# Kernel optimization log

Measured on AMD Instinct MI355X. Metric: run time of the kernel, lower is better.

Reference implementation:

```python
import jax, jax.numpy as jnp
import numpy as np

KH = KW = 3
K = KH * KW
MAX_S, MIN_S = 3.0, 0.5
A_S = (MAX_S - MIN_S) / 2.0   # 1.25
B_S = (MAX_S + MIN_S) / 2.0   # 1.75


def _conv3x3(x, w, b):
    # x: [B,C,H,W], w: [O,C,3,3], b: [O]
    y = jax.lax.conv_general_dilated(
        x, w, window_strides=(1, 1), padding='SAME',
        dimension_numbers=('NCHW', 'OIHW', 'NCHW'))
    return y + b[None, :, None, None]


def setup_inputs() -> dict:
    key = jax.random.key(0)
    ks = jax.random.split(key, 6)
    b, c_in, c_out, h, w = 2, 64, 64, 192, 192
    x = jax.random.normal(ks[0], (b, c_in, h, w), jnp.float32)
    w_main = jax.random.normal(ks[1], (c_out, c_in, KH, KW), jnp.float32) * 0.05
    # offset-branch params (randomized, small, so offsets are non-trivial)
    w_rot = jax.random.normal(ks[2], (2, c_in, 3, 3), jnp.float32) * 0.05
    b_rot = jnp.array([0.0, 1.0], jnp.float32)  # init_angle=0 -> (sin,cos)=(0,1)
    w_str = jax.random.normal(ks[3], (1, c_in, 3, 3), jnp.float32) * 0.05
    b_str = jnp.zeros((1,), jnp.float32)
    w_whole = jax.random.normal(ks[4], (1, c_in, 3, 3), jnp.float32) * 0.05
    b_whole = jnp.zeros((1,), jnp.float32)
    return dict(x=x, w_main=w_main, w_rot=w_rot, b_rot=b_rot,
                w_str=w_str, b_str=b_str, w_whole=w_whole, b_whole=b_whole)


def reference(x, w_main, w_rot, b_rot, w_str, b_str, w_whole, b_whole):
    bsz, cin, H, W = x.shape
    # base kernel offsets (row-major over 3x3, centered): di rows, dj cols
    di = jnp.array([-1, -1, -1, 0, 0, 0, 1, 1, 1], jnp.float32)  # [K]
    dj = jnp.array([-1, 0, 1, -1, 0, 1, -1, 0, 1], jnp.float32)  # [K]

    # per-pixel rotation (normalized sin/cos)
    rot = _conv3x3(x, w_rot, b_rot)          # [B,2,H,W]
    sin, cos = rot[:, 0], rot[:, 1]          # [B,H,W]
    norm = jnp.sqrt(sin * sin + cos * cos + 1e-6)
    sin, cos = sin / norm, cos / norm

    # stretch on the row coordinate, bounded by tanh into [MIN_S, MAX_S]
    r = jnp.tanh(_conv3x3(x, w_str, b_str))[:, 0] * A_S + B_S   # [B,H,W]
    # whole-grid rescale >= 1
    wr = 1.0 + jax.nn.relu(_conv3x3(x, w_whole, b_whole))[:, 0]  # [B,H,W]

    # banded offsets before rotation: row comp scaled by r*wr, col by wr
    bd0 = di * (r * wr)[..., None]           # [B,H,W,K]
    bd1 = dj * wr[..., None]                 # [B,H,W,K]
    # rotation matrix [[cos, sin], [-sin, cos]] @ [bd0; bd1], minus base
    off_y = cos[..., None] * bd0 + sin[..., None] * bd1 - di     # [B,H,W,K]
    off_x = -sin[..., None] * bd0 + cos[..., None] * bd1 - dj    # [B,H,W,K]

    # sampling positions: p = out_pos - pad + tap + offset; (tap - pad) == di/dj
    py = jnp.arange(H, dtype=jnp.float32)[None, :, None, None] + di + off_y
    px = jnp.arange(W, dtype=jnp.float32)[None, None, :, None] + dj + off_x

    # bilinear gather with zero padding outside the image
    x_bhwc = x.transpose(0, 2, 3, 1)         # [B,H,W,C]
    y0 = jnp.floor(py)
    x0 = jnp.floor(px)
    ty = py - y0
    tx = px - x0
    y0i = y0.astype(jnp.int32)
    x0i = x0.astype(jnp.int32)
    bidx = jnp.arange(bsz)[:, None, None, None]

    def gather(yi, xi):
        valid = ((yi >= 0) & (yi < H) & (xi >= 0) & (xi < W)).astype(x.dtype)
        v = x_bhwc[bidx, jnp.clip(yi, 0, H - 1), jnp.clip(xi, 0, W - 1)]  # [B,H,W,K,C]
        return v * valid[..., None]

    sampled = (gather(y0i, x0i) * ((1 - ty) * (1 - tx))[..., None]
               + gather(y0i, x0i + 1) * ((1 - ty) * tx)[..., None]
               + gather(y0i + 1, x0i) * (ty * (1 - tx))[..., None]
               + gather(y0i + 1, x0i + 1) * (ty * tx)[..., None])  # [B,H,W,K,C]

    w_flat = w_main.reshape(w_main.shape[0], w_main.shape[1], K)   # [O,C,K]
    out = jnp.einsum('bhwkc,ock->bohw', sampled, w_flat)
    return out
```

## Files before the change

kernel.cpp:

```cpp
#include <hip/hip_runtime.h>
#include <hip/hip_bf16.h>
#include <stdint.h>

typedef unsigned short u16;
typedef unsigned int   u32;

#define HH 192
#define WW 192
#define HWSZ (192*192)
#define NPIX (2*HWSZ)
#define NTILE 1152
#define TPB   144

typedef __attribute__((ext_vector_type(8))) short short8;
typedef __attribute__((ext_vector_type(4))) float floatx4;

__device__ __forceinline__ float bflo(u32 u){ union{u32 i; float f;} v; v.i = u<<16; return v.f; }
__device__ __forceinline__ float bfhi(u32 u){ union{u32 i; float f;} v; v.i = u & 0xffff0000u; return v.f; }
__device__ __forceinline__ float bf2f(u16 u){ union{u32 i; float f;} v; v.i = ((u32)u)<<16; return v.f; }
__device__ __forceinline__ u16 f2bf(float f){
    union{float f; u32 i;} v; v.f = f;
    u32 b = v.i;
    u32 r = b + 0x7fffu + ((b>>16)&1u);
    return (u16)(r>>16);
}
__device__ __forceinline__ u32 pkbf(float a, float b){
    __hip_bfloat162 h = __float22bfloat162_rn(make_float2(a, b));
    union { __hip_bfloat162 h; u32 u; } cv; cv.h = h; return cv.u;
}

__device__ __forceinline__ int band_tile(int blk){ return (blk & 7)*TPB + (blk >> 3); }

__device__ __forceinline__ int sniff_fp32(const void* x) {
    const u32* x32 = (const u32*)x;
    int l = threadIdx.x & 63;
    u32 v = x32[l*2];
    u32 e = (v >> 7) & 0xFFu;
    int vote = (e >= 0x60u && e <= 0x8Fu) ? 1 : 0;
    unsigned long long m = __ballot(vote);
    return (__popcll(m) < 40) ? 1 : 0;
}

__device__ __forceinline__ u16 pick16(const void* p, int i, int fp32) {
    return fp32 ? f2bf(((const float*)p)[i]) : ((const u16*)p)[i];
}
__device__ __forceinline__ float pickf(const void* p, int i, int fp32) {
    return fp32 ? ((const float*)p)[i] : bf2f(((const u16*)p)[i]);
}

__global__ __launch_bounds__(256) void k0_prep(const void* __restrict__ x,
                        const void* __restrict__ wm,
                        const void* __restrict__ wrot,
                        const void* __restrict__ brot,
                        const void* __restrict__ wstr,
                        const void* __restrict__ bstr,
                        const void* __restrict__ wwh,
                        const void* __restrict__ bwh,
                        u16* __restrict__ bfrag, float* __restrict__ wf) {
    int fp32 = sniff_fp32(x);
    int e = blockIdx.x*256 + threadIdx.x;
    if (e < 9*2*4*64*8) {
        int j    = e & 7;
        int lane = (e>>3) & 63;
        int wd   = (e>>9) & 3;
        int kk   = (e>>11) & 1;
        int k    = e>>12;
        int o = wd*16 + (lane & 15);
        int c = kk*32 + ((lane>>4)&3)*8 + j;
        bfrag[e] = pick16(wm, (o*64 + c)*9 + k, fp32);
    }
    if (e < 9216) {
        int j   = e & 3;
        int rem = e >> 2;
        int tap = rem % 9;
        int c   = rem / 9;
        float s;
        if (j==0)      s = pickf(wrot, c*9 + tap, fp32);
        else if (j==1) s = pickf(wrot, (64+c)*9 + tap, fp32);
        else if (j==2) s = pickf(wstr, c*9 + tap, fp32);
        else           s = pickf(wwh,  c*9 + tap, fp32);
        wf[e] = s;
    }
    if (e < 4) {
        float bv;
        if (e==0)      bv = pickf(brot, 0, fp32);
        else if (e==1) bv = pickf(brot, 1, fp32);
        else if (e==2) bv = pickf(bstr, 0, fp32);
        else           bv = pickf(bwh,  0, fp32);
        wf[9216 + e] = bv;
    }
}

__global__ __launch_bounds__(256) void k1_transpose(const void* __restrict__ x, u16* __restrict__ xt) {
    int fp32 = sniff_fp32(x);
    int t = threadIdx.x;
    int g = t >> 6, p = t & 63;
    int tile = band_tile(blockIdx.x);
    int gp = tile*64 + p;
    int b = gp / HWSZ, hw = gp % HWSZ;
    u32 v[8];
    if (fp32) {
        const float* src = (const float*)x + (size_t)(b*64 + g*16)*HWSZ + hw;
#pragma unroll
        for (int i = 0; i < 8; i++) {
            float a = src[(size_t)(2*i)*HWSZ];
            float c = src[(size_t)(2*i+1)*HWSZ];
            v[i] = pkbf(a, c);
        }
    } else {
        const u16* src = (const u16*)x + (size_t)(b*64 + g*16)*HWSZ + hw;
#pragma unroll
        for (int i = 0; i < 8; i++) {
            u32 a = src[(size_t)(2*i)*HWSZ];
            u32 c = src[(size_t)(2*i+1)*HWSZ];
            v[i] = a | (c<<16);
        }
    }
    uint4* dst = (uint4*)(xt + (size_t)gp*64 + g*16);
    dst[0] = make_uint4(v[0], v[1], v[2], v[3]);
    dst[1] = make_uint4(v[4], v[5], v[6], v[7]);
}

__global__ __launch_bounds__(256) void k2_fields(const void* __restrict__ x, const float* __restrict__ wf,
                          float4* __restrict__ fields) {
    __shared__ float4 red[256];
    int fp32 = sniff_fp32(x);
    int t = threadIdx.x;
    int q = t >> 6, p = t & 63;
    int gp0 = band_tile(blockIdx.x) * 64;
    int gp = gp0 + p;
    int b = gp / HWSZ, hw = gp % HWSZ;
    int h = hw / WW, w = hw % WW;
    float a0=0.f, a1=0.f, a2=0.f, a3=0.f;
    const float4* wf4 = (const float4*)wf;
    if (fp32) {
        const float* xf = (const float*)x;
#pragma unroll 2
        for (int c16 = 0; c16 < 16; c16++) {
            int c = q*16 + c16;
            size_t plane = (size_t)(b*64 + c)*HWSZ;
#pragma unroll
            for (int kh = 0; kh < 3; kh++) {
                int y = h + kh - 1;
                if ((unsigned)y >= (unsigned)HH) continue;
#pragma unroll
                for (int kw = 0; kw < 3; kw++) {
                    int xx = w + kw - 1;
                    if ((unsigned)xx >= (unsigned)WW) continue;
                    float v = xf[plane + (size_t)y*WW + xx];
                    float4 wv = wf4[c*9 + kh*3 + kw];
                    a0 = fmaf(v, wv.x, a0);
                    a1 = fmaf(v, wv.y, a1);
                    a2 = fmaf(v, wv.z, a2);
                    a3 = fmaf(v, wv.w, a3);
                }
            }
        }
    } else {
        const u16* xu = (const u16*)x;
#pragma unroll 2
        for (int c16 = 0; c16 < 16; c16++) {
            int c = q*16 + c16;
            size_t plane = (size_t)(b*64 + c)*HWSZ;
#pragma unroll
            for (int kh = 0; kh < 3; kh++) {
                int y = h + kh - 1;
                if ((unsigned)y >= (unsigned)HH) continue;
#pragma unroll
                for (int kw = 0; kw < 3; kw++) {
                    int xx = w + kw - 1;
                    if ((unsigned)xx >= (unsigned)WW) continue;
                    float v = bf2f(xu[plane + (size_t)y*WW + xx]);
                    float4 wv = wf4[c*9 + kh*3 + kw];
                    a0 = fmaf(v, wv.x, a0);
                    a1 = fmaf(v, wv.y, a1);
                    a2 = fmaf(v, wv.z, a2);
                    a3 = fmaf(v, wv.w, a3);
                }
            }
        }
    }
    red[t] = make_float4(a0, a1, a2, a3);
    __syncthreads();
    if (t < 64) {
        float4 r0 = red[t], r1 = red[t+64], r2 = red[t+128], r3 = red[t+192];
        float s0 = r0.x + r1.x + r2.x + r3.x;
        float s1 = r0.y + r1.y + r2.y + r3.y;
        float s2 = r0.z + r1.z + r2.z + r3.z;
        float s3 = r0.w + r1.w + r2.w + r3.w;
        float sr = s0 + wf[9216];
        float cr = s1 + wf[9217];
        float inv = 1.0f / sqrtf(sr*sr + cr*cr + 1e-6f);
        float r  = tanhf(s2 + wf[9218])*1.25f + 1.75f;
        float wrv = 1.0f + fmaxf(s3 + wf[9219], 0.0f);
        fields[gp0 + t] = make_float4(sr*inv, cr*inv, r*wrv, wrv);
    }
}

__device__ __forceinline__ void load16(const u16* base, u32 r[8]) {
    const uint4* p = (const uint4*)base;
    uint4 a = p[0], b = p[1];
    r[0]=a.x; r[1]=a.y; r[2]=a.z; r[3]=a.w;
    r[4]=b.x; r[5]=b.y; r[6]=b.z; r[7]=b.w;
}

__global__ __launch_bounds__(256) void k3_main(const void* __restrict__ xorig,
                                               const u16* __restrict__ xt,
                                               const float4* __restrict__ fields,
                                               const u16* __restrict__ bfrag,
                                               void* __restrict__ out) {
    __shared__ u16 samp[2][64*72];

    int fp32 = sniff_fp32(xorig);
    int t = threadIdx.x;
    int pix0 = band_tile(blockIdx.x) * 64;
    int b   = pix0 / HWSZ;
    int hw0 = pix0 % HWSZ;

    int p = t >> 2, q = t & 3;
    int hw = hw0 + p;
    int h = hw / WW, w = hw % WW;
    float4 f = fields[pix0 + p];
    float sn = f.x, cs = f.y, rwr = f.z, wr = f.w;
    const u16* xbase = xt + (size_t)b*HWSZ*64;

    int wd = t >> 6, lane = t & 63;
    int quad = lane >> 4, l15 = lane & 15;
    floatx4 acc[4];
#pragma unroll
    for (int i=0;i<4;i++) acc[i] = (floatx4){0.f,0.f,0.f,0.f};
    const short8* bfr = (const short8*)bfrag;

    u32 r00[8], r01[8], r10[8], r11[8];
    float w00, w01, w10, w11;

    auto coords_load = [&](int k) {
        int di = k/3 - 1;
        int dj = k%3 - 1;
        float bd0 = (float)di * rwr;
        float bd1 = (float)dj * wr;
        float py = (float)h + cs*bd0 + sn*bd1;
        float px = (float)w - sn*bd0 + cs*bd1;
        float y0f = floorf(py), x0f = floorf(px);
        float ty = py - y0f, tx = px - x0f;
        int y0 = (int)y0f, x0 = (int)x0f;
        int y1 = y0 + 1,   x1 = x0 + 1;
        float fy0 = ((unsigned)y0 < (unsigned)HH) ? 1.f : 0.f;
        float fy1 = ((unsigned)y1 < (unsigned)HH) ? 1.f : 0.f;
        float fx0 = ((unsigned)x0 < (unsigned)WW) ? 1.f : 0.f;
        float fx1 = ((unsigned)x1 < (unsigned)WW) ? 1.f : 0.f;
        int yc0 = min(max(y0,0),HH-1), yc1 = min(max(y1,0),HH-1);
        int xc0 = min(max(x0,0),WW-1), xc1 = min(max(x1,0),WW-1);
        w00 = (1.f-ty)*(1.f-tx)*fy0*fx0;
        w01 = (1.f-ty)*tx      *fy0*fx1;
        w10 = ty      *(1.f-tx)*fy1*fx0;
        w11 = ty      *tx      *fy1*fx1;
        const u16* row0 = xbase + (size_t)(yc0*WW)*64 + q*16;
        const u16* row1 = xbase + (size_t)(yc1*WW)*64 + q*16;
        load16(row0 + xc0*64, r00);
        load16(row0 + xc1*64, r01);
        load16(row1 + xc0*64, r10);
        load16(row1 + xc1*64, r11);
    };

    auto blend_store = [&](int buf) {
        u32 packed[8];
#pragma unroll
        for (int d=0; d<8; d++) {
            float s0 = w00*bflo(r00[d]) + w01*bflo(r01[d]) + w10*bflo(r10[d]) + w11*bflo(r11[d]);
            float s1 = w00*bfhi(r00[d]) + w01*bfhi(r01[d]) + w10*bfhi(r10[d]) + w11*bfhi(r11[d]);
            packed[d] = pkbf(s0, s1);
        }
        uint4* dst = (uint4*)&samp[buf][p*72 + q*16];
        dst[0] = make_uint4(packed[0],packed[1],packed[2],packed[3]);
        dst[1] = make_uint4(packed[4],packed[5],packed[6],packed[7]);
    };

    coords_load(0);
    blend_store(0);

#pragma unroll 1
    for (int k = 0; k < 9; k++) {
        __syncthreads();
        if (k < 8) coords_load(k+1);
        short8 b0 = bfr[((k*2+0)*4 + wd)*64 + lane];
        short8 b1 = bfr[((k*2+1)*4 + wd)*64 + lane];
        const u16* sb = samp[k & 1];
#pragma unroll
        for (int mt=0; mt<4; mt++) {
            int pr = mt*16 + l15;
            short8 a0 = *(const short8*)&sb[pr*72 +      quad*8];
            short8 a1 = *(const short8*)&sb[pr*72 + 32 + quad*8];
            acc[mt] = __builtin_amdgcn_mfma_f32_16x16x32_bf16(a0, b0, acc[mt], 0, 0, 0);
            acc[mt] = __builtin_amdgcn_mfma_f32_16x16x32_bf16(a1, b1, acc[mt], 0, 0, 0);
        }
        if (k < 8) blend_store((k+1) & 1);
    }
    __syncthreads();

    {
        int o = wd*16 + l15;
#pragma unroll
        for (int mt=0; mt<4; mt++)
#pragma unroll
            for (int rg=0; rg<4; rg++) {
                int pxi = mt*16 + quad*4 + rg;
                samp[0][o*72 + pxi] = f2bf(acc[mt][rg]);
            }
    }
    __syncthreads();
    {
        int o = t >> 2, q2 = t & 3;
        const uint4* s = (const uint4*)&samp[0][o*72 + q2*16];
        uint4 v0 = s[0], v1 = s[1];
        size_t base = (size_t)(b*64 + o)*HWSZ + hw0 + q2*16;
        if (fp32) {
            float4* df = (float4*)((float*)out + base);
            df[0] = make_float4(bflo(v0.x), bfhi(v0.x), bflo(v0.y), bfhi(v0.y));
            df[1] = make_float4(bflo(v0.z), bfhi(v0.z), bflo(v0.w), bfhi(v0.w));
            df[2] = make_float4(bflo(v1.x), bfhi(v1.x), bflo(v1.y), bfhi(v1.y));
            df[3] = make_float4(bflo(v1.z), bfhi(v1.z), bflo(v1.w), bfhi(v1.w));
        } else {
            uint4* du = (uint4*)((u16*)out + base);
            du[0] = v0; du[1] = v1;
        }
    }
}

extern "C" void kernel_launch(void* const* d_in, const int* in_sizes, int n_in,
                              void* d_out, int out_size, void* d_ws, size_t ws_size,
                              hipStream_t stream) {
    const void* x    = d_in[0];
    const void* wm   = d_in[1];
    const void* wrot = d_in[2];
    const void* brot = d_in[3];
    const void* wstr = d_in[4];
    const void* bstr = d_in[5];
    const void* wwh  = d_in[6];
    const void* bwh  = d_in[7];

    char* ws = (char*)d_ws;
    u16*    xt     = (u16*)   (ws);
    float4* fields = (float4*)(ws + 9437184);
    u16*    bfrag  = (u16*)   (ws + 10616832);
    float*  wf     = (float*) (ws + 10690560);

    k0_prep     <<<dim3(144),   dim3(256), 0, stream>>>(x, wm, wrot, brot, wstr, bstr, wwh, bwh, bfrag, wf);
    k1_transpose<<<dim3(NTILE), dim3(256), 0, stream>>>(x, xt);
    k2_fields   <<<dim3(NTILE), dim3(256), 0, stream>>>(x, wf, fields);
    k3_main     <<<dim3(NTILE), dim3(256), 0, stream>>>(x, xt, (const float4*)fields, bfrag, d_out);
}
```

Before: 152.0 us.

## Build MFMA A-fragments directly in registers, removing LDS staging of sampled data

Each wave now owns 16 pixels and every lane gathers and bilinearly blends the channels that map straight onto its MFMA A-operand layout, so the sampled tile no longer goes through shared memory and the per-tap __syncthreads are gone. Each wave loops over all four output-channel tiles, loading B fragments from global memory, where before each wave handled one output tile and read A from LDS. Corner loads are double-buffered in registers for the next tap. In exchange register pressure rises (two sets of eight uint4 plus weights), which may lower occupancy, and B-fragment traffic per wave grows fourfold.

```diff
diff --git a/kernel.cpp b/kernel.cpp
--- a/kernel.cpp
+++ b/kernel.cpp
@@ -62,10 +62,10 @@
     if (e < 9*2*4*64*8) {
         int j    = e & 7;
         int lane = (e>>3) & 63;
-        int wd   = (e>>9) & 3;
+        int nt   = (e>>9) & 3;
         int kk   = (e>>11) & 1;
         int k    = e>>12;
-        int o = wd*16 + (lane & 15);
+        int o = nt*16 + (lane & 15);
         int c = kk*32 + ((lane>>4)&3)*8 + j;
         bfrag[e] = pick16(wm, (o*64 + c)*9 + k, fp32);
     }
@@ -197,19 +197,12 @@
     }
 }
 
-__device__ __forceinline__ void load16(const u16* base, u32 r[8]) {
-    const uint4* p = (const uint4*)base;
-    uint4 a = p[0], b = p[1];
-    r[0]=a.x; r[1]=a.y; r[2]=a.z; r[3]=a.w;
-    r[4]=b.x; r[5]=b.y; r[6]=b.z; r[7]=b.w;
-}
-
 __global__ __launch_bounds__(256) void k3_main(const void* __restrict__ xorig,
                                                const u16* __restrict__ xt,
                                                const float4* __restrict__ fields,
                                                const u16* __restrict__ bfrag,
                                                void* __restrict__ out) {
-    __shared__ u16 samp[2][64*72];
+    __shared__ u16 cmat[64*72];
 
     int fp32 = sniff_fp32(xorig);
     int t = threadIdx.x;
@@ -217,24 +210,24 @@
     int b   = pix0 / HWSZ;
     int hw0 = pix0 % HWSZ;
 
-    int p = t >> 2, q = t & 3;
-    int hw = hw0 + p;
+    int wv = t >> 6, lane = t & 63;
+    int quad = lane >> 4, l15 = lane & 15;
+    int pl = wv*16 + l15;
+    int hw = hw0 + pl;
     int h = hw / WW, w = hw % WW;
-    float4 f = fields[pix0 + p];
+    float4 f = fields[pix0 + pl];
     float sn = f.x, cs = f.y, rwr = f.z, wr = f.w;
-    const u16* xbase = xt + (size_t)b*HWSZ*64;
-
-    int wd = t >> 6, lane = t & 63;
-    int quad = lane >> 4, l15 = lane & 15;
+    const u16* xbase = xt + (size_t)b*HWSZ*64 + quad*8;
+
     floatx4 acc[4];
 #pragma unroll
     for (int i=0;i<4;i++) acc[i] = (floatx4){0.f,0.f,0.f,0.f};
     const short8* bfr = (const short8*)bfrag;
 
-    u32 r00[8], r01[8], r10[8], r11[8];
-    float w00, w01, w10, w11;
-
-    auto coords_load = [&](int k) {
+    uint4 cr[2][8];
+    float wg[2][4];
+
+    auto coords_load = [&](int k, int buf) {
         int di = k/3 - 1;
         int dj = k%3 - 1;
         float bd0 = (float)di * rwr;
@@ -251,67 +244,73 @@
         float fx1 = ((unsigned)x1 < (unsigned)WW) ? 1.f : 0.f;
         int yc0 = min(max(y0,0),HH-1), yc1 = min(max(y1,0),HH-1);
         int xc0 = min(max(x0,0),WW-1), xc1 = min(max(x1,0),WW-1);
-        w00 = (1.f-ty)*(1.f-tx)*fy0*fx0;
-        w01 = (1.f-ty)*tx      *fy0*fx1;
-        w10 = ty      *(1.f-tx)*fy1*fx0;
-        w11 = ty      *tx      *fy1*fx1;
-        const u16* row0 = xbase + (size_t)(yc0*WW)*64 + q*16;
-        const u16* row1 = xbase + (size_t)(yc1*WW)*64 + q*16;
-        load16(row0 + xc0*64, r00);
-        load16(row0 + xc1*64, r01);
-        load16(row1 + xc0*64, r10);
-        load16(row1 + xc1*64, r11);
+        wg[buf][0] = (1.f-ty)*(1.f-tx)*fy0*fx0;
+        wg[buf][1] = (1.f-ty)*tx      *fy0*fx1;
+        wg[buf][2] = ty      *(1.f-tx)*fy1*fx0;
+        wg[buf][3] = ty      *tx      *fy1*fx1;
+        const u16* p00 = xbase + (size_t)(yc0*WW + xc0)*64;
+        const u16* p01 = xbase + (size_t)(yc0*WW + xc1)*64;
+        const u16* p10 = xbase + (size_t)(yc1*WW + xc0)*64;
+        const u16* p11 = xbase + (size_t)(yc1*WW + xc1)*64;
+        cr[buf][0] = *(const uint4*)(p00);
+        cr[buf][1] = *(const uint4*)(p00 + 32);
+        cr[buf][2] = *(const uint4*)(p01);
+        cr[buf][3] = *(const uint4*)(p01 + 32);
+        cr[buf][4] = *(const uint4*)(p10);
+        cr[buf][5] = *(const uint4*)(p10 + 32);
+        cr[buf][6] = *(const uint4*)(p11);
+        cr[buf][7] = *(const uint4*)(p11 + 32);
     };
 
-    auto blend_store = [&](int buf) {
-        u32 packed[8];
-#pragma unroll
-        for (int d=0; d<8; d++) {
-            float s0 = w00*bflo(r00[d]) + w01*bflo(r01[d]) + w10*bflo(r10[d]) + w11*bflo(r11[d]);
-            float s1 = w00*bfhi(r00[d]) + w01*bfhi(r01[d]) + w10*bfhi(r10[d]) + w11*bfhi(r11[d]);
-            packed[d] = pkbf(s0, s1);
-        }
-        uint4* dst = (uint4*)&samp[buf][p*72 + q*16];
-        dst[0] = make_uint4(packed[0],packed[1],packed[2],packed[3]);
-        dst[1] = make_uint4(packed[4],packed[5],packed[6],packed[7]);
-    };
-
-    coords_load(0);
-    blend_store(0);
+    coords_load(0, 0);
 
 #pragma unroll 1
     for (int k = 0; k < 9; k++) {
-        __syncthreads();
-        if (k < 8) coords_load(k+1);
-        short8 b0 = bfr[((k*2+0)*4 + wd)*64 + lane];
-        short8 b1 = bfr[((k*2+1)*4 + wd)*64 + lane];
-        const u16* sb = samp[k & 1];
-#pragma unroll
-        for (int mt=0; mt<4; mt++) {
-            int pr = mt*16 + l15;
-            short8 a0 = *(const short8*)&sb[pr*72 +      quad*8];
-            short8 a1 = *(const short8*)&sb[pr*72 + 32 + quad*8];
-            acc[mt] = __builtin_amdgcn_mfma_f32_16x16x32_bf16(a0, b0, acc[mt], 0, 0, 0);
-            acc[mt] = __builtin_amdgcn_mfma_f32_16x16x32_bf16(a1, b1, acc[mt], 0, 0, 0);
-        }
-        if (k < 8) blend_store((k+1) & 1);
-    }
-    __syncthreads();
-
-    {
-        int o = wd*16 + l15;
-#pragma unroll
-        for (int mt=0; mt<4; mt++)
-#pragma unroll
-            for (int rg=0; rg<4; rg++) {
-                int pxi = mt*16 + quad*4 + rg;
-                samp[0][o*72 + pxi] = f2bf(acc[mt][rg]);
+        int buf = k & 1;
+        float w00 = wg[buf][0], w01 = wg[buf][1], w10 = wg[buf][2], w11 = wg[buf][3];
+        u32 a0u[4], a1u[4];
+        {
+            const u32* c00 = (const u32*)&cr[buf][0];
+            const u32* c01 = (const u32*)&cr[buf][2];
+            const u32* c10 = (const u32*)&cr[buf][4];
+            const u32* c11 = (const u32*)&cr[buf][6];
+#pragma unroll
+            for (int j = 0; j < 4; j++) {
+                float s0 = w00*bflo(c00[j]) + w01*bflo(c01[j]) + w10*bflo(c10[j]) + w11*bflo(c11[j]);
+                float s1 = w00*bfhi(c00[j]) + w01*bfhi(c01[j]) + w10*bfhi(c10[j]) + w11*bfhi(c11[j]);
+                a0u[j] = pkbf(s0, s1);
+                float t0 = w00*bflo(c00[j+4]) + w01*bflo(c01[j+4]) + w10*bflo(c10[j+4]) + w11*bflo(c11[j+4]);
+                float t1 = w00*bfhi(c00[j+4]) + w01*bfhi(c01[j+4]) + w10*bfhi(c10[j+4]) + w11*bfhi(c11[j+4]);
+                a1u[j] = pkbf(t0, t1);
             }
+        }
+        short8 a0 = *(short8*)a0u;
+        short8 a1 = *(short8*)a1u;
+
+        if (k < 8) coords_load(k+1, buf ^ 1);
+
+#pragma unroll
+        for (int nt = 0; nt < 4; nt++) {
+            short8 b0 = bfr[((k*2+0)*4 + nt)*64 + lane];
+            short8 b1 = bfr[((k*2+1)*4 + nt)*64 + lane];
+            acc[nt] = __builtin_amdgcn_mfma_f32_16x16x32_bf16(a0, b0, acc[nt], 0, 0, 0);
+            acc[nt] = __builtin_amdgcn_mfma_f32_16x16x32_bf16(a1, b1, acc[nt], 0, 0, 0);
+        }
+    }
+
+#pragma unroll
+    for (int nt = 0; nt < 4; nt++) {
+        int o = nt*16 + l15;
+#pragma unroll
+        for (int rg = 0; rg < 4; rg++) {
+            int pxi = wv*16 + quad*4 + rg;
+            cmat[o*72 + pxi] = f2bf(acc[nt][rg]);
+        }
     }
     __syncthreads();
     {
         int o = t >> 2, q2 = t & 3;
-        const uint4* s = (const uint4*)&samp[0][o*72 + q2*16];
+        const uint4* s = (const uint4*)&cmat[o*72 + q2*16];
         uint4 v0 = s[0], v1 = s[1];
         size_t base = (size_t)(b*64 + o)*HWSZ + hw0 + q2*16;
         if (fp32) {
```

Result: slower. 248.7 us (+63.6%).
